# Optimization experiments

Measured on AMD Instinct MI355X. Metric: run time of the kernel, lower is better.

Reference implementation:

```python
import jax, jax.numpy as jnp
import numpy as np

# DeepSpeed FixedSparsityConfig defaults (attention='unidirectional')
BLOCK = 16
NUM_LOCAL_BLOCKS = 4   # local window = 4 blocks = 64 tokens
D_MODEL = 1024
N_HEADS = 16
HEAD_DIM = D_MODEL // N_HEADS


def _block_layout(seq_len: int) -> np.ndarray:
    """Token-level boolean mask [S,S] from the fixed unidirectional block layout.
    Allowed iff: (same 4-block local window AND block_k <= block_q) OR
                 (block_k % 4 == 3 AND block_k <= block_q)  (causal global column).
    Same layout for every head (different_layout_per_head=False)."""
    nb = seq_len // BLOCK
    r = np.arange(nb)
    causal = r[None, :] <= r[:, None]
    same_win = (r[:, None] // NUM_LOCAL_BLOCKS) == (r[None, :] // NUM_LOCAL_BLOCKS)
    glob = (r[None, :] % NUM_LOCAL_BLOCKS) == (NUM_LOCAL_BLOCKS - 1)
    layout = (same_win & causal) | (glob & causal)
    return np.kron(layout, np.ones((BLOCK, BLOCK), dtype=bool))


def setup_inputs() -> dict:
    key = jax.random.key(0)
    ks = jax.random.split(key, 7)
    B, S = 2, 2048
    init = 1.0 / np.sqrt(D_MODEL)
    x = jax.random.normal(ks[0], (B, S, D_MODEL), jnp.float32)
    key_padding_mask = jnp.zeros((B, S), jnp.float32)  # additive mask ('add' mode)
    Wq = jax.random.normal(ks[1], (D_MODEL, D_MODEL), jnp.float32) * init
    Wk = jax.random.normal(ks[2], (D_MODEL, D_MODEL), jnp.float32) * init
    Wv = jax.random.normal(ks[3], (D_MODEL, D_MODEL), jnp.float32) * init
    bq = jax.random.normal(ks[4], (D_MODEL,), jnp.float32) * 0.01
    bk = jax.random.normal(ks[5], (D_MODEL,), jnp.float32) * 0.01
    bv = jax.random.normal(ks[6], (D_MODEL,), jnp.float32) * 0.01
    return dict(x=x, key_padding_mask=key_padding_mask,
                Wq=Wq, bq=bq, Wk=Wk, bk=bk, Wv=Wv, bv=bv)


def reference(x, key_padding_mask, Wq, bq, Wk, bk, Wv, bv):
    B, S, D = x.shape
    q = (x @ Wq + bq).reshape(B, S, N_HEADS, HEAD_DIM)
    k = (x @ Wk + bk).reshape(B, S, N_HEADS, HEAD_DIM)
    v = (x @ Wv + bv).reshape(B, S, N_HEADS, HEAD_DIM)
    scale = HEAD_DIM ** -0.5  # DeepSpeed scales by head_size**-0.5 inside softmax
    scores = jnp.einsum('bqhd,bkhd->bhqk', q, k) * scale
    scores = scores + key_padding_mask[:, None, None, :]
    mask = jnp.asarray(_block_layout(S))  # [S,S] bool; absent blocks excluded from softmax
    scores = jnp.where(mask[None, None], scores, -jnp.inf)
    attn = jax.nn.softmax(scores, axis=-1)
    out = jnp.einsum('bhqk,bkhd->bqhd', attn, v)
    return out.reshape(B, S, D)
```

## Files before the change

kernel.cpp:

```cpp
#include <hip/hip_runtime.h>
#include <hip/hip_bf16.h>

typedef __bf16 bf16;
typedef __bf16 bf16x4 __attribute__((ext_vector_type(4)));
typedef __bf16 bf16x8 __attribute__((ext_vector_type(8)));
typedef float  f32x4  __attribute__((ext_vector_type(4)));

#define D_MODEL 1024
#define S_LEN   2048
#define BATCH   2
#define NH      16
#define HD      64
#define NX ((size_t)BATCH * S_LEN * D_MODEL)
#define NROWS (BATCH * S_LEN)

__device__ inline void gl_lds16(const bf16* g, bf16* l) {
    __builtin_amdgcn_global_load_lds(
        (const __attribute__((address_space(1))) void*)g,
        (__attribute__((address_space(3))) void*)l, 16, 0, 0);
}

__global__ __launch_bounds__(256) void cvt_all(
    const float* __restrict__ x,
    const float* __restrict__ Wq, const float* __restrict__ Wk,
    const float* __restrict__ Wv,
    bf16* __restrict__ xb, bf16* __restrict__ Wt)
{
    if (blockIdx.x < 2048) {
        const size_t base = ((size_t)blockIdx.x * 256 + threadIdx.x) * 8;
        const float4 a = *(const float4*)(x + base);
        const float4 b = *(const float4*)(x + base + 4);
        bf16x8 o;
        o[0] = (bf16)a.x; o[1] = (bf16)a.y; o[2] = (bf16)a.z; o[3] = (bf16)a.w;
        o[4] = (bf16)b.x; o[5] = (bf16)b.y; o[6] = (bf16)b.z; o[7] = (bf16)b.w;
        *(bf16x8*)(xb + base) = o;
        return;
    }
    const int id = blockIdx.x - 2048;
    const int z = id / 256, tid = id % 256;
    const int k0 = (tid >> 4) * 64, n0 = (tid & 15) * 64;
    const float* W = (z == 0) ? Wq : (z == 1) ? Wk : Wv;

    __shared__ bf16 tile[64 * 72];
    const int r16 = threadIdx.x >> 4, c4 = (threadIdx.x & 15) << 2;

#pragma unroll
    for (int rr = 0; rr < 4; ++rr) {
        const int row = rr * 16 + r16;
        const float4 v = *(const float4*)(W + (size_t)(k0 + row) * D_MODEL + n0 + c4);
        bf16x4 o; o[0] = (bf16)v.x; o[1] = (bf16)v.y; o[2] = (bf16)v.z; o[3] = (bf16)v.w;
        *(bf16x4*)(tile + row * 72 + c4) = o;
    }
    __syncthreads();
#pragma unroll
    for (int rr = 0; rr < 4; ++rr) {
        const int row = rr * 16 + r16;
        bf16x4 o;
#pragma unroll
        for (int j = 0; j < 4; ++j) o[j] = tile[(c4 + j) * 72 + row];
        *(bf16x4*)(Wt + (size_t)(z * D_MODEL + n0 + row) * D_MODEL + k0 + c4) = o;
    }
}

__global__ __launch_bounds__(256) void zero_acc(float* __restrict__ p)
{
    const size_t i = ((size_t)blockIdx.x * 256 + threadIdx.x) * 4;
    *(float4*)(p + i) = make_float4(0.f, 0.f, 0.f, 0.f);
}

__global__ __launch_bounds__(256) void gemm_bt(
    const bf16* __restrict__ Xb, const bf16* __restrict__ Wt,
    const float* __restrict__ bq, const float* __restrict__ bk,
    const float* __restrict__ bv, bf16* __restrict__ QKV)
{
    const int id  = blockIdx.y * gridDim.x + blockIdx.x;
    const int xcd = id & 7, rem = id >> 3;
    const int ntile = xcd * 3 + (rem % 3), mtile = rem / 3;
    const int n0 = ntile * 128, m0 = mtile * 128;
    const int z  = n0 >> 10;
    const float* bias = (z == 0) ? bq : (z == 1) ? bk : bv;
    const float scale = (z == 0) ? 0.125f : 1.0f;
    bf16* C = QKV + (size_t)z * NX;
    const int ncol0 = n0 & 1023;

    __shared__ bf16 As[128 * 32];
    __shared__ bf16 Bs[128 * 32];
    __shared__ bf16 Es[4][16 * 66];

    const int t = threadIdx.x, wave = t >> 6, lane = t & 63;
    const int wm = wave >> 1, wn = wave & 1;
    const int col = lane & 15, quad = lane >> 4;
    const int srow = t >> 2, sc8 = (t & 3) << 3;

    f32x4 acc[4][4] = {};

    for (int k0 = 0; k0 < D_MODEL; k0 += 32) {
        gl_lds16(Xb + (size_t)(m0 + srow) * D_MODEL + k0 + sc8,      As + wave * 512);
        gl_lds16(Xb + (size_t)(m0 + 64 + srow) * D_MODEL + k0 + sc8, As + 2048 + wave * 512);
        gl_lds16(Wt + (size_t)(n0 + srow) * D_MODEL + k0 + sc8,      Bs + wave * 512);
        gl_lds16(Wt + (size_t)(n0 + 64 + srow) * D_MODEL + k0 + sc8, Bs + 2048 + wave * 512);
        __syncthreads();

        bf16x8 a[4], b[4];
#pragma unroll
        for (int mt = 0; mt < 4; ++mt)
            a[mt] = *(const bf16x8*)(As + (wm * 64 + mt * 16 + col) * 32 + quad * 8);
#pragma unroll
        for (int nt = 0; nt < 4; ++nt)
            b[nt] = *(const bf16x8*)(Bs + (wn * 64 + nt * 16 + col) * 32 + quad * 8);
#pragma unroll
        for (int mt = 0; mt < 4; ++mt)
#pragma unroll
            for (int nt = 0; nt < 4; ++nt)
                acc[mt][nt] = __builtin_amdgcn_mfma_f32_16x16x32_bf16(a[mt], b[nt], acc[mt][nt], 0, 0, 0);
        __syncthreads();
    }

    bf16* E = Es[wave];
    const int r8 = lane >> 3, c8 = (lane & 7) << 3;
#pragma unroll
    for (int mt = 0; mt < 4; ++mt) {
#pragma unroll
        for (int nt = 0; nt < 4; ++nt) {
            const float bsv = bias[ncol0 + wn * 64 + nt * 16 + col];
#pragma unroll
            for (int i = 0; i < 4; ++i)
                E[(quad * 4 + i) * 66 + nt * 16 + col] =
                    (bf16)((acc[mt][nt][i] + bsv) * scale);
        }
#pragma unroll
        for (int ph = 0; ph < 2; ++ph) {
            const int row = ph * 8 + r8;
            const bf16x8 v = *(const bf16x8*)(E + row * 66 + c8);
            const int rg = m0 + wm * 64 + mt * 16 + row;
            *(bf16x8*)(C + (size_t)rg * D_MODEL + ncol0 + wn * 64 + c8) = v;
        }
    }
}

__global__ __launch_bounds__(256) void sparse_attn_part(
    const bf16* __restrict__ Q, const bf16* __restrict__ Kv,
    const bf16* __restrict__ Vv, const float* __restrict__ kpm,
    float* __restrict__ Oacc, float* __restrict__ L)
{
    const int hb = blockIdx.y, h = hb >> 1, b = hb & 1;
    const int t = threadIdx.x, wavei = t >> 6, lane = t & 63;
    const int col = lane & 15, quad = lane >> 4;

    int w = 0, c0 = 0, c1 = 1;
    {
        int x = blockIdx.x, acc = 0;
        for (int wd = 0; wd < 32; ++wd) {
            const int wc = 31 - wd;
            const int ni = ((wc + 3) >> 2) + 1;
            const int np = (ni + 3) >> 2;
            if (x < acc + np) {
                w = wc;
                const int p = x - acc;
                c0 = p * 4;
                c1 = (c0 + 4 < ni) ? (c0 + 4) : ni;
                break;
            }
            acc += np;
        }
    }
    const int qb = 4 * w + wavei;
    const int nGlob = (w + 3) >> 2;

    __shared__ bf16 KbS[2][64 * 72];
    __shared__ bf16 VtS[2][64 * 72];
    __shared__ bf16 Ps[4][16 * 72];

    const size_t qrow = ((size_t)(b * S_LEN + qb * 16 + col)) * D_MODEL + h * HD;
    const bf16x8 aq0 = *(const bf16x8*)(Q + qrow + quad * 8);
    const bf16x8 aq1 = *(const bf16x8*)(Q + qrow + 32 + quad * 8);

    f32x4 o[4] = {};
    float lacc[4] = {0.f, 0.f, 0.f, 0.f};

    const int srow = t >> 2, sd16 = (t & 3) << 4;
    const int sg = srow >> 4, sr = srow & 15;
    const int p2 = t & 31, dg8 = (t >> 5) << 3;
    const int key0 = 2 * p2, vg = key0 >> 4, vr = key0 & 15;

    auto kb_of = [&](int it, int g) -> int {
        if (it == nGlob) return 4 * w + g;
        const int j = 4 * it + g;
        return (j < w) ? (4 * j + 3) : 3;
    };

    bf16x8 rk0, rk1, rv0, rv1;
    {
        const size_t krow = ((size_t)(b * S_LEN + kb_of(c0, sg) * 16 + sr)) * D_MODEL + h * HD + sd16;
        rk0 = *(const bf16x8*)(Kv + krow);
        rk1 = *(const bf16x8*)(Kv + krow + 8);
        const size_t vrow = ((size_t)(b * S_LEN + kb_of(c0, vg) * 16 + vr)) * D_MODEL + h * HD + dg8;
        rv0 = *(const bf16x8*)(Vv + vrow);
        rv1 = *(const bf16x8*)(Vv + vrow + D_MODEL);
        bf16* Kb = KbS[c0 & 1];
        bf16* Vt = VtS[c0 & 1];
        *(bf16x8*)(Kb + srow * 72 + sd16)     = rk0;
        *(bf16x8*)(Kb + srow * 72 + sd16 + 8) = rk1;
#pragma unroll
        for (int j = 0; j < 8; ++j) {
            bf16 pr[2] = { rv0[j], rv1[j] };
            *(unsigned int*)(Vt + (dg8 + j) * 72 + key0) = *(unsigned int*)pr;
        }
    }

    for (int it = c0; it < c1; ++it) {
        __syncthreads();
        const int cur = it & 1, nxt = cur ^ 1;
        const bool more = (it + 1 < c1);
        if (more) {
            const size_t krow = ((size_t)(b * S_LEN + kb_of(it + 1, sg) * 16 + sr)) * D_MODEL + h * HD + sd16;
            rk0 = *(const bf16x8*)(Kv + krow);
            rk1 = *(const bf16x8*)(Kv + krow + 8);
            const size_t vrow = ((size_t)(b * S_LEN + kb_of(it + 1, vg) * 16 + vr)) * D_MODEL + h * HD + dg8;
            rv0 = *(const bf16x8*)(Vv + vrow);
            rv1 = *(const bf16x8*)(Vv + vrow + D_MODEL);
        }
        const bf16* Kb = KbS[cur];
        const bf16* Vt = VtS[cur];

        f32x4 s[4];
        float mval[4];
        bool  val[4];
#pragma unroll
        for (int g = 0; g < 4; ++g) {
            int kb;
            if (it == nGlob) { kb = 4 * w + g; val[g] = (g <= wavei); }
            else { const int j = 4 * it + g; val[g] = (j < w); kb = val[g] ? (4 * j + 3) : 3; }
            mval[g] = kpm[b * S_LEN + kb * 16 + col];
            f32x4 zz = {};
            const bf16x8 bk0 = *(const bf16x8*)(Kb + (g * 16 + col) * 72 + quad * 8);
            const bf16x8 bk1 = *(const bf16x8*)(Kb + (g * 16 + col) * 72 + 32 + quad * 8);
            zz = __builtin_amdgcn_mfma_f32_16x16x32_bf16(aq0, bk0, zz, 0, 0, 0);
            s[g] = __builtin_amdgcn_mfma_f32_16x16x32_bf16(aq1, bk1, zz, 0, 0, 0);
        }

#pragma unroll
        for (int i = 0; i < 4; ++i) {
#pragma unroll
            for (int g = 0; g < 4; ++g) {
                const float si = val[g] ? (s[g][i] + mval[g]) : -1e30f;
                const float pv = __expf(si);
                lacc[i] += pv;
                Ps[wavei][(quad * 4 + i) * 72 + g * 16 + col] = (bf16)pv;
            }
        }

        const bf16x8 aP0 = *(const bf16x8*)(Ps[wavei] + col * 72 + quad * 8);
        const bf16x8 aP1 = *(const bf16x8*)(Ps[wavei] + col * 72 + 32 + quad * 8);
#pragma unroll
        for (int nt = 0; nt < 4; ++nt) {
            const bf16x8 b0 = *(const bf16x8*)(Vt + (nt * 16 + col) * 72 + quad * 8);
            const bf16x8 b1 = *(const bf16x8*)(Vt + (nt * 16 + col) * 72 + 32 + quad * 8);
            o[nt] = __builtin_amdgcn_mfma_f32_16x16x32_bf16(aP0, b0, o[nt], 0, 0, 0);
            o[nt] = __builtin_amdgcn_mfma_f32_16x16x32_bf16(aP1, b1, o[nt], 0, 0, 0);
        }

        if (more) {
            bf16* KbN = KbS[nxt];
            bf16* VtN = VtS[nxt];
            *(bf16x8*)(KbN + srow * 72 + sd16)     = rk0;
            *(bf16x8*)(KbN + srow * 72 + sd16 + 8) = rk1;
#pragma unroll
            for (int j = 0; j < 8; ++j) {
                bf16 pr[2] = { rv0[j], rv1[j] };
                *(unsigned int*)(VtN + (dg8 + j) * 72 + key0) = *(unsigned int*)pr;
            }
        }
    }

#pragma unroll
    for (int i = 0; i < 4; ++i) {
        float rs = lacc[i];
        rs += __shfl_xor(rs, 1);
        rs += __shfl_xor(rs, 2);
        rs += __shfl_xor(rs, 4);
        rs += __shfl_xor(rs, 8);
        const int rg = b * S_LEN + qb * 16 + quad * 4 + i;
        if (col == 0) atomicAdd(L + rg * NH + h, rs);
#pragma unroll
        for (int nt = 0; nt < 4; ++nt)
            atomicAdd(Oacc + (size_t)rg * D_MODEL + h * HD + nt * 16 + col, o[nt][i]);
    }
}

__global__ __launch_bounds__(256) void normalize_out(
    const float* __restrict__ Oacc, const float* __restrict__ L,
    float* __restrict__ out)
{
    const size_t i4 = ((size_t)blockIdx.x * 256 + threadIdx.x) * 4;
    const int rg = (int)(i4 >> 10);
    const int h  = ((int)i4 & 1023) >> 6;
    const float inv = 1.0f / L[rg * NH + h];
    float4 v = *(const float4*)(Oacc + i4);
    v.x *= inv; v.y *= inv; v.z *= inv; v.w *= inv;
    *(float4*)(out + i4) = v;
}

extern "C" void kernel_launch(void* const* d_in, const int* in_sizes, int n_in,
                              void* d_out, int out_size, void* d_ws, size_t ws_size,
                              hipStream_t stream)
{
    const float* x = nullptr; const float* kpm = nullptr;
    const float* Wp[3] = {nullptr, nullptr, nullptr};
    const float* bp[3] = {nullptr, nullptr, nullptr};
    int wn = 0, bn = 0;
    for (int i = 0; i < n_in; ++i) {
        const float* p = (const float*)d_in[i];
        const long s = in_sizes[i];
        if (s == (long)NX)            x = p;
        else if (s == BATCH * S_LEN)  kpm = p;
        else if (s == D_MODEL * D_MODEL && wn < 3) Wp[wn++] = p;
        else if (s == D_MODEL && bn < 3)           bp[bn++] = p;
    }

    bf16*  Qb   = (bf16*)d_ws;
    bf16*  Kb   = Qb + NX;
    bf16*  Vb   = Kb + NX;
    float* Oacc = (float*)(Vb + NX);
    bf16* Xb = (bf16*)d_out;
    bf16* Wt = Xb + NX;
    float* outp = (float*)d_out;

    cvt_all<<<2048 + 768, 256, 0, stream>>>(x, Wp[0], Wp[1], Wp[2], Xb, Wt);

    zero_acc<<<(int)((NX + (size_t)NROWS * NH) / 4 / 256), 256, 0, stream>>>(Oacc);

    gemm_bt<<<dim3(24, 32), 256, 0, stream>>>(Xb, Wt, bp[0], bp[1], bp[2], Qb);

    sparse_attn_part<<<dim3(54, NH * BATCH), 256, 0, stream>>>(
        Qb, Kb, Vb, kpm, Oacc, Oacc + NX);

    normalize_out<<<(int)(NX / 4 / 256), 256, 0, stream>>>(Oacc, Oacc + NX, outp);
}
```

Baseline: 165.9 us.

## Write single-partition attention rows directly and normalize only multi-partition rows

Query windows whose keys fit in one partition (w<=12) now normalize and write the output directly instead of using atomics into an accumulator. Zeroing and normalization are restricted to rows 832..2047, which are split across partitions. The zeroing is folded into the conversion kernel, removing one launch. This cuts atomic traffic and the full-size zero and normalize passes. The cost is extra index logic and a hard-coded row boundary tied to the partition scheme.

```diff
diff --git a/kernel.cpp b/kernel.cpp
--- a/kernel.cpp
+++ b/kernel.cpp
@@ -13,6 +13,8 @@
 #define HD      64
 #define NX ((size_t)BATCH * S_LEN * D_MODEL)
 #define NROWS (BATCH * S_LEN)
+#define MPROW0 832
+#define MPROWS 1216
 
 __device__ inline void gl_lds16(const bf16* g, bf16* l) {
     __builtin_amdgcn_global_load_lds(
@@ -24,7 +26,8 @@
     const float* __restrict__ x,
     const float* __restrict__ Wq, const float* __restrict__ Wk,
     const float* __restrict__ Wv,
-    bf16* __restrict__ xb, bf16* __restrict__ Wt)
+    bf16* __restrict__ xb, bf16* __restrict__ Wt,
+    float* __restrict__ Oacc, float* __restrict__ L)
 {
     if (blockIdx.x < 2048) {
         const size_t base = ((size_t)blockIdx.x * 256 + threadIdx.x) * 8;
@@ -36,36 +39,47 @@
         *(bf16x8*)(xb + base) = o;
         return;
     }
-    const int id = blockIdx.x - 2048;
-    const int z = id / 256, tid = id % 256;
-    const int k0 = (tid >> 4) * 64, n0 = (tid & 15) * 64;
-    const float* W = (z == 0) ? Wq : (z == 1) ? Wk : Wv;
-
-    __shared__ bf16 tile[64 * 72];
-    const int r16 = threadIdx.x >> 4, c4 = (threadIdx.x & 15) << 2;
-
-#pragma unroll
-    for (int rr = 0; rr < 4; ++rr) {
-        const int row = rr * 16 + r16;
-        const float4 v = *(const float4*)(W + (size_t)(k0 + row) * D_MODEL + n0 + c4);
-        bf16x4 o; o[0] = (bf16)v.x; o[1] = (bf16)v.y; o[2] = (bf16)v.z; o[3] = (bf16)v.w;
-        *(bf16x4*)(tile + row * 72 + c4) = o;
-    }
-    __syncthreads();
-#pragma unroll
-    for (int rr = 0; rr < 4; ++rr) {
-        const int row = rr * 16 + r16;
-        bf16x4 o;
-#pragma unroll
-        for (int j = 0; j < 4; ++j) o[j] = tile[(c4 + j) * 72 + row];
-        *(bf16x4*)(Wt + (size_t)(z * D_MODEL + n0 + row) * D_MODEL + k0 + c4) = o;
-    }
-}
-
-__global__ __launch_bounds__(256) void zero_acc(float* __restrict__ p)
-{
-    const size_t i = ((size_t)blockIdx.x * 256 + threadIdx.x) * 4;
-    *(float4*)(p + i) = make_float4(0.f, 0.f, 0.f, 0.f);
+    if (blockIdx.x < 2816) {
+        const int id = blockIdx.x - 2048;
+        const int z = id / 256, tid = id % 256;
+        const int k0 = (tid >> 4) * 64, n0 = (tid & 15) * 64;
+        const float* W = (z == 0) ? Wq : (z == 1) ? Wk : Wv;
+
+        __shared__ bf16 tile[64 * 72];
+        const int r16 = threadIdx.x >> 4, c4 = (threadIdx.x & 15) << 2;
+
+#pragma unroll
+        for (int rr = 0; rr < 4; ++rr) {
+            const int row = rr * 16 + r16;
+            const float4 v = *(const float4*)(W + (size_t)(k0 + row) * D_MODEL + n0 + c4);
+            bf16x4 o; o[0] = (bf16)v.x; o[1] = (bf16)v.y; o[2] = (bf16)v.z; o[3] = (bf16)v.w;
+            *(bf16x4*)(tile + row * 72 + c4) = o;
+        }
+        __syncthreads();
+#pragma unroll
+        for (int rr = 0; rr < 4; ++rr) {
+            const int row = rr * 16 + r16;
+            bf16x4 o;
+#pragma unroll
+            for (int j = 0; j < 4; ++j) o[j] = tile[(c4 + j) * 72 + row];
+            *(bf16x4*)(Wt + (size_t)(z * D_MODEL + n0 + row) * D_MODEL + k0 + c4) = o;
+        }
+        return;
+    }
+    if (blockIdx.x < 5248) {
+        const int g   = (blockIdx.x - 2816) * 256 + threadIdx.x;
+        const int b   = g / (MPROWS * 256);
+        const int rem = g % (MPROWS * 256);
+        const int row = MPROW0 + (rem >> 8);
+        const int c4  = (rem & 255) << 2;
+        const size_t off = (size_t)(b * S_LEN + row) * D_MODEL + c4;
+        *(float4*)(Oacc + off) = make_float4(0.f, 0.f, 0.f, 0.f);
+        return;
+    }
+    {
+        const int g = (blockIdx.x - 5248) * 256 + threadIdx.x;
+        *(float4*)(L + (size_t)g * 4) = make_float4(0.f, 0.f, 0.f, 0.f);
+    }
 }
 
 __global__ __launch_bounds__(256) void gemm_bt(
@@ -141,7 +155,8 @@
 __global__ __launch_bounds__(256) void sparse_attn_part(
     const bf16* __restrict__ Q, const bf16* __restrict__ Kv,
     const bf16* __restrict__ Vv, const float* __restrict__ kpm,
-    float* __restrict__ Oacc, float* __restrict__ L)
+    float* __restrict__ Oacc, float* __restrict__ L,
+    float* __restrict__ out)
 {
     const int hb = blockIdx.y, h = hb >> 1, b = hb & 1;
     const int t = threadIdx.x, wavei = t >> 6, lane = t & 63;
@@ -166,6 +181,7 @@
     }
     const int qb = 4 * w + wavei;
     const int nGlob = (w + 3) >> 2;
+    const bool single = (w <= 12);
 
     __shared__ bf16 KbS[2][64 * 72];
     __shared__ bf16 VtS[2][64 * 72];
@@ -273,32 +289,52 @@
         }
     }
 
-#pragma unroll
-    for (int i = 0; i < 4; ++i) {
-        float rs = lacc[i];
-        rs += __shfl_xor(rs, 1);
-        rs += __shfl_xor(rs, 2);
-        rs += __shfl_xor(rs, 4);
-        rs += __shfl_xor(rs, 8);
-        const int rg = b * S_LEN + qb * 16 + quad * 4 + i;
-        if (col == 0) atomicAdd(L + rg * NH + h, rs);
-#pragma unroll
-        for (int nt = 0; nt < 4; ++nt)
-            atomicAdd(Oacc + (size_t)rg * D_MODEL + h * HD + nt * 16 + col, o[nt][i]);
-    }
-}
-
-__global__ __launch_bounds__(256) void normalize_out(
+    if (single) {
+#pragma unroll
+        for (int i = 0; i < 4; ++i) {
+            float rs = lacc[i];
+            rs += __shfl_xor(rs, 1);
+            rs += __shfl_xor(rs, 2);
+            rs += __shfl_xor(rs, 4);
+            rs += __shfl_xor(rs, 8);
+            const float inv = 1.0f / rs;
+            const int rg = b * S_LEN + qb * 16 + quad * 4 + i;
+#pragma unroll
+            for (int nt = 0; nt < 4; ++nt)
+                out[(size_t)rg * D_MODEL + h * HD + nt * 16 + col] = o[nt][i] * inv;
+        }
+    } else {
+#pragma unroll
+        for (int i = 0; i < 4; ++i) {
+            float rs = lacc[i];
+            rs += __shfl_xor(rs, 1);
+            rs += __shfl_xor(rs, 2);
+            rs += __shfl_xor(rs, 4);
+            rs += __shfl_xor(rs, 8);
+            const int rg = b * S_LEN + qb * 16 + quad * 4 + i;
+            if (col == 0) atomicAdd(L + rg * NH + h, rs);
+#pragma unroll
+            for (int nt = 0; nt < 4; ++nt)
+                atomicAdd(Oacc + (size_t)rg * D_MODEL + h * HD + nt * 16 + col, o[nt][i]);
+        }
+    }
+}
+
+__global__ __launch_bounds__(256) void normalize_mp(
     const float* __restrict__ Oacc, const float* __restrict__ L,
     float* __restrict__ out)
 {
-    const size_t i4 = ((size_t)blockIdx.x * 256 + threadIdx.x) * 4;
-    const int rg = (int)(i4 >> 10);
-    const int h  = ((int)i4 & 1023) >> 6;
-    const float inv = 1.0f / L[rg * NH + h];
-    float4 v = *(const float4*)(Oacc + i4);
+    const int g   = blockIdx.x * 256 + threadIdx.x;
+    const int b   = g / (MPROWS * 256);
+    const int rem = g % (MPROWS * 256);
+    const int row = MPROW0 + (rem >> 8);
+    const int c4  = (rem & 255) << 2;
+    const int rg  = b * S_LEN + row;
+    const float inv = 1.0f / L[rg * NH + (c4 >> 6)];
+    const size_t off = (size_t)rg * D_MODEL + c4;
+    float4 v = *(const float4*)(Oacc + off);
     v.x *= inv; v.y *= inv; v.z *= inv; v.w *= inv;
-    *(float4*)(out + i4) = v;
+    *(float4*)(out + off) = v;
 }
 
 extern "C" void kernel_launch(void* const* d_in, const int* in_sizes, int n_in,
@@ -322,18 +358,17 @@
     bf16*  Kb   = Qb + NX;
     bf16*  Vb   = Kb + NX;
     float* Oacc = (float*)(Vb + NX);
+    float* Lp   = Oacc + NX;
     bf16* Xb = (bf16*)d_out;
     bf16* Wt = Xb + NX;
     float* outp = (float*)d_out;
 
-    cvt_all<<<2048 + 768, 256, 0, stream>>>(x, Wp[0], Wp[1], Wp[2], Xb, Wt);
-
-    zero_acc<<<(int)((NX + (size_t)NROWS * NH) / 4 / 256), 256, 0, stream>>>(Oacc);
+    cvt_all<<<5312, 256, 0, stream>>>(x, Wp[0], Wp[1], Wp[2], Xb, Wt, Oacc, Lp);
 
     gemm_bt<<<dim3(24, 32), 256, 0, stream>>>(Xb, Wt, bp[0], bp[1], bp[2], Qb);
 
     sparse_attn_part<<<dim3(54, NH * BATCH), 256, 0, stream>>>(
-        Qb, Kb, Vb, kpm, Oacc, Oacc + NX);
-
-    normalize_out<<<(int)(NX / 4 / 256), 256, 0, stream>>>(Oacc, Oacc + NX, outp);
-}
+        Qb, Kb, Vb, kpm, Oacc, Lp, outp);
+
+    normalize_mp<<<(BATCH * MPROWS * 256) / 256, 256, 0, stream>>>(Oacc, Lp, outp);
+}
```

Result: faster. 160.6 us (-3.2%).
